# Kernel optimization log

Measured on AMD Instinct MI355X. Metric: run time of the kernel, lower is better.

The kernel has to match this reference:

```python
import jax, jax.numpy as jnp
import numpy as np

H = 1024       # hidden_size
NH = 16        # num heads
HD = H // NH   # head dim
EPS = 1e-12


def setup_inputs() -> dict:
    key = jax.random.key(0)
    ks = jax.random.split(key, 12)
    s = 1.0 / np.sqrt(H)
    return {
        "hidden_states": jax.random.normal(ks[0], (2, 2048, H), jnp.float32),
        "attention_mask": jnp.zeros((2, 1, 1, 2048), jnp.float32),
        "wq": jax.random.uniform(ks[1], (H, H), jnp.float32, -s, s),
        "bq": jnp.zeros((H,), jnp.float32),
        "wk": jax.random.uniform(ks[2], (H, H), jnp.float32, -s, s),
        "bk": jnp.zeros((H,), jnp.float32),
        "wv": jax.random.uniform(ks[3], (H, H), jnp.float32, -s, s),
        "bv": jnp.zeros((H,), jnp.float32),
        "wo": jax.random.uniform(ks[4], (H, H), jnp.float32, -s, s),
        "bo": jnp.zeros((H,), jnp.float32),
        "ln_gamma": jnp.ones((H,), jnp.float32),
        "ln_beta": jnp.zeros((H,), jnp.float32),
    }


def reference(hidden_states, attention_mask, wq, bq, wk, bk, wv, bv, wo, bo, ln_gamma, ln_beta):
    residual = hidden_states
    # pre-LayerNorm
    mu = jnp.mean(hidden_states, axis=-1, keepdims=True)
    var = jnp.var(hidden_states, axis=-1, keepdims=True)
    x = (hidden_states - mu) / jnp.sqrt(var + EPS) * ln_gamma + ln_beta

    B, S, _ = x.shape
    # QKV projections (torch Linear: x @ W.T + b), split heads -> [B, NH, S, HD]
    def proj(w, b):
        return (x @ w.T + b).reshape(B, S, NH, HD).transpose(0, 2, 1, 3)
    q = proj(wq, bq)
    k = proj(wk, bk)
    v = proj(wv, bv)

    scores = jnp.einsum("bhqd,bhkd->bhqk", q, k) / np.sqrt(HD).astype(np.float32)
    scores = scores + attention_mask  # broadcast additive mask
    probs = jax.nn.softmax(scores, axis=-1)
    ctx = jnp.einsum("bhqk,bhkd->bhqd", probs, v)
    ctx = ctx.transpose(0, 2, 1, 3).reshape(B, S, NH * HD)

    out = ctx @ wo.T + bo
    return out + residual
```

## Files before the change

### kernel.cpp

```cpp
#include <hip/hip_runtime.h>
#include <cstdint>

typedef unsigned short u16;
typedef __bf16  bf16x8 __attribute__((ext_vector_type(8)));
typedef unsigned short u16x8 __attribute__((ext_vector_type(8)));
typedef unsigned short u16x4 __attribute__((ext_vector_type(4)));
typedef float   f32x4  __attribute__((ext_vector_type(4)));

#define LOG2E 1.44269504088896340736f

__device__ __forceinline__ u16 f2b(float f) {
  union { __bf16 h; u16 u; } c; c.h = (__bf16)f;
  return c.u;
}

__device__ __forceinline__ int swz(int row) { return (row & 7) ^ ((row >> 3) & 7); }
__device__ __forceinline__ int sidx(int row, int k) {
  return row * 64 + ((((k >> 3) ^ swz(row)) & 7) << 3) + (k & 7);
}
__device__ __forceinline__ bf16x8 ld_frag(const u16* base, int row, int k) {
  return *(const bf16x8*)(base + sidx(row, k));
}

__device__ __forceinline__ void async16(const u16* g, u16* l) {
  __builtin_amdgcn_global_load_lds(
      (__attribute__((address_space(1))) unsigned int*)(uintptr_t)g,
      (__attribute__((address_space(3))) unsigned int*)(uintptr_t)l,
      16, 0, 0);
}

__device__ __forceinline__ void plswap32(unsigned int &a, unsigned int &b) {
  auto r = __builtin_amdgcn_permlane32_swap(a, b, false, false);
  a = r[0]; b = r[1];
}
__device__ __forceinline__ void plswap16(unsigned int &a, unsigned int &b) {
#if __has_builtin(__builtin_amdgcn_permlane16_swap)
  auto r = __builtin_amdgcn_permlane16_swap(a, b, false, false);
  a = r[0]; b = r[1];
#else
  asm volatile("v_permlane16_swap_b32 %0, %1" : "+v"(a), "+v"(b));
#endif
}

__global__ __launch_bounds__(256) void prep_kernel(
    const float* __restrict__ hs, const float* __restrict__ gamma,
    const float* __restrict__ beta, u16* __restrict__ X,
    const float* __restrict__ w0, const float* __restrict__ w1,
    const float* __restrict__ w2, const float* __restrict__ w3,
    u16* __restrict__ Wd) {
  const int tid = threadIdx.x;
  if (blockIdx.x >= 4096) {
    const int idx4 = blockIdx.x - 4096;
    const int mat = idx4 >> 10;
    const float* src = (mat == 0) ? w0 : (mat == 1) ? w1 : (mat == 2) ? w2 : w3;
    const int idx = ((idx4 & 1023) * 256 + tid) * 4;
    f32x4 v = *(const f32x4*)(src + idx);
    u16x4 o;
#pragma unroll
    for (int j = 0; j < 4; ++j) o[j] = f2b(v[j]);
    *(u16x4*)(Wd + (size_t)mat * 1048576 + idx) = o;
    return;
  }
  __shared__ float red[8];
  const int row = blockIdx.x;
  f32x4 v = *(const f32x4*)(hs + (size_t)row * 1024 + tid * 4);
  float s = 0.f, s2 = 0.f;
#pragma unroll
  for (int j = 0; j < 4; ++j) { s += v[j]; s2 += v[j] * v[j]; }
#pragma unroll
  for (int o = 1; o < 64; o <<= 1) { s += __shfl_xor(s, o); s2 += __shfl_xor(s2, o); }
  const int wid = tid >> 6, lane = tid & 63;
  if (lane == 0) { red[wid] = s; red[4 + wid] = s2; }
  __syncthreads();
  s  = red[0] + red[1] + red[2] + red[3];
  s2 = red[4] + red[5] + red[6] + red[7];
  const float mean = s * (1.f / 1024.f);
  const float var  = fmaxf(s2 * (1.f / 1024.f) - mean * mean, 0.f);
  const float rstd = rsqrtf(var + 1e-12f);
  f32x4 g = *(const f32x4*)(gamma + tid * 4);
  f32x4 bb = *(const f32x4*)(beta + tid * 4);
  u16x4 outv;
#pragma unroll
  for (int j = 0; j < 4; ++j) outv[j] = f2b((v[j] - mean) * rstd * g[j] + bb[j]);
  *(u16x4*)(X + (size_t)row * 1024 + tid * 4) = outv;
}

template <int MODE>
__device__ __forceinline__ void gemm_tile_128(
    const u16* __restrict__ A, const u16* __restrict__ Bt,
    const float* __restrict__ bias, const float* __restrict__ res,
    void* __restrict__ Cv, int ldc, int m0, int nG) {
  __shared__ __align__(16) u16 As[128 * 64];
  __shared__ __align__(16) u16 Bs[128 * 64];
  const int tid = threadIdx.x;
  const int wid = tid >> 6;
  const int lane = tid & 63;
  const int l15 = lane & 15, lq = lane >> 4;
  const int wm = (wid & 1) << 6, wn = (wid >> 1) << 6;
  const int srow = tid >> 3;
  const int sg = tid & 7;

  f32x4 acc[4][4] = {};
  u16x8 ar[4], br[4];

#pragma unroll
  for (int i = 0; i < 4; ++i) {
    int row = (i << 5) + srow;
    ar[i] = *(const u16x8*)(A  + (size_t)row * 1024 + (sg << 3));
    br[i] = *(const u16x8*)(Bt + (size_t)row * 1024 + (sg << 3));
  }

  for (int k0 = 0; k0 < 1024; k0 += 64) {
    if (k0) __syncthreads();
#pragma unroll
    for (int i = 0; i < 4; ++i) {
      int row = (i << 5) + srow;
      *(u16x8*)(As + sidx(row, sg << 3)) = ar[i];
      *(u16x8*)(Bs + sidx(row, sg << 3)) = br[i];
    }
    __syncthreads();
    if (k0 + 64 < 1024) {
#pragma unroll
      for (int i = 0; i < 4; ++i) {
        int row = (i << 5) + srow;
        ar[i] = *(const u16x8*)(A  + (size_t)row * 1024 + k0 + 64 + (sg << 3));
        br[i] = *(const u16x8*)(Bt + (size_t)row * 1024 + k0 + 64 + (sg << 3));
      }
    }
#pragma unroll
    for (int kk = 0; kk < 2; ++kk) {
      bf16x8 af[4], bf[4];
#pragma unroll
      for (int mi = 0; mi < 4; ++mi) af[mi] = ld_frag(As, wm + (mi << 4) + l15, (kk << 5) + (lq << 3));
#pragma unroll
      for (int ni = 0; ni < 4; ++ni) bf[ni] = ld_frag(Bs, wn + (ni << 4) + l15, (kk << 5) + (lq << 3));
#pragma unroll
      for (int mi = 0; mi < 4; ++mi)
#pragma unroll
        for (int ni = 0; ni < 4; ++ni)
          acc[mi][ni] = __builtin_amdgcn_mfma_f32_16x16x32_bf16(af[mi], bf[ni], acc[mi][ni], 0, 0, 0);
    }
  }
  __syncthreads();

  if (MODE == 2) {
    u16* Rg = (wid < 2 ? As : Bs) + ((wid & 1) << 12);
#pragma unroll
    for (int ni = 0; ni < 4; ++ni) {
      const float bv = bias[wn + (ni << 4) + l15];
#pragma unroll
      for (int mi = 0; mi < 4; ++mi) {
        u16x4 pk;
#pragma unroll
        for (int r = 0; r < 4; ++r) pk[r] = f2b(acc[mi][ni][r] + bv);
        *(u16x4*)(Rg + sidx((ni << 4) + l15, (mi << 4) + (lq << 2))) = pk;
      }
    }
    __asm__ volatile("" ::: "memory");
    const int rrow = lane >> 3;
    const int rg8  = (lane & 7) << 3;
    const int mg0 = m0 + wm;
    const int bb = mg0 >> 11, ss0 = mg0 & 2047;
    const int hh = (nG + wn) >> 6;
    u16* vbase = (u16*)Cv + ((size_t)((bb << 4) + hh) * 64) * 2048 + ss0;
#pragma unroll
    for (int p = 0; p < 8; ++p) {
      const int nl = (p << 3) + rrow;
      bf16x8 rowv = ld_frag(Rg, nl, rg8);
      *(bf16x8*)(vbase + (size_t)nl * 2048 + rg8) = rowv;
    }
  } else {
#pragma unroll
    for (int ni = 0; ni < 4; ++ni) {
      const int n = wn + (ni << 4) + l15;
      const float bv = bias[n];
#pragma unroll
      for (int mi = 0; mi < 4; ++mi) {
#pragma unroll
        for (int r = 0; r < 4; ++r) {
          const int m = wm + (mi << 4) + (lq << 2) + r;
          float v = acc[mi][ni][r] + bv;
          if (MODE == 1) {
            v += res[(size_t)m * ldc + n];
            ((float*)Cv)[(size_t)m * ldc + n] = v;
          } else {
            ((u16*)Cv)[(size_t)m * ldc + n] = f2b(v);
          }
        }
      }
    }
  }
}

__global__ __launch_bounds__(256, 3) void qkv_kernel(
    const u16* __restrict__ X, const u16* __restrict__ W,
    const float* __restrict__ bq, const float* __restrict__ bk, const float* __restrict__ bv,
    u16* __restrict__ QK, u16* __restrict__ VT) {
  const int n0 = blockIdx.x << 7;
  const int m0 = blockIdx.y << 7;
  const int wsel = n0 >> 10;
  const int nloc = n0 & 1023;
  const u16* Bt = W + (size_t)wsel * 1048576 + (size_t)nloc * 1024;
  if (wsel < 2) {
    const float* bias = (wsel == 0 ? bq : bk) + nloc;
    gemm_tile_128<0>(X + (size_t)m0 * 1024, Bt, bias, nullptr,
                     QK + (size_t)m0 * 2048 + n0, 2048, 0, 0);
  } else {
    gemm_tile_128<2>(X + (size_t)m0 * 1024, Bt, bv + nloc, nullptr,
                     VT, 0, m0, nloc);
  }
}

__global__ __launch_bounds__(256, 3) void out_kernel(
    const u16* __restrict__ CTX, const u16* __restrict__ wo,
    const float* __restrict__ bo, const float* __restrict__ res, float* __restrict__ OUT) {
  const int n0 = blockIdx.x << 7;
  const int m0 = blockIdx.y << 7;
  gemm_tile_128<1>(CTX + (size_t)m0 * 1024, wo + (size_t)n0 * 1024, bo + n0,
                   res + (size_t)m0 * 1024 + n0, OUT + (size_t)m0 * 1024 + n0, 1024, 0, 0);
}

__global__ __launch_bounds__(256, 2) void attn_kernel(
    const u16* __restrict__ QK, const u16* __restrict__ VT,
    const float* __restrict__ mask, u16* __restrict__ CTX) {
  __shared__ __align__(16) u16 Ksb[2][64 * 64];
  __shared__ __align__(16) u16 Vtsb[2][64 * 64];
  const int tid = threadIdx.x;
  const int wid = tid >> 6;
  const int lane = tid & 63;
  const int l15 = lane & 15, lq = lane >> 4;

  const int lid = blockIdx.x;
  const int sw = ((lid & 7) << 6) | (lid >> 3);
  const int qt = sw & 15;
  const int hz = sw >> 4;
  const int h = hz & 15;
  const int b = hz >> 4;

  const int qbase = (b << 11) + (qt << 7) + (wid << 5);
  const u16* Kbase  = QK + (size_t)(b << 11) * 2048 + 1024 + (h << 6);
  const u16* VTbase = VT + (size_t)(((b << 4) + h) << 6) * 2048;

  bf16x8 qf[2][2];
#pragma unroll
  for (int f = 0; f < 2; ++f)
#pragma unroll
    for (int kc = 0; kc < 2; ++kc)
      qf[f][kc] = *(const bf16x8*)(QK + (size_t)(qbase + (f << 4) + l15) * 2048 + (h << 6) + (kc << 5) + (lq << 3));

  f32x4 cacc[2][4] = {};
  float l_run[2] = {0.f, 0.f};

  const int sg = lane & 7;
  const int srow0 = (wid << 4) + (lane >> 3);
  const int srow1 = srow0 + 8;
  const int gk0 = ((sg ^ swz(srow0)) & 7) << 3;
  const int gk1 = ((sg ^ swz(srow1)) & 7) << 3;
  const int ld0 = ((wid << 1) + 0) << 9;
  const int ld1 = ((wid << 1) + 1) << 9;

  async16(Kbase + (size_t)srow0 * 2048 + gk0, &Ksb[0][0] + ld0);
  async16(Kbase + (size_t)srow1 * 2048 + gk1, &Ksb[0][0] + ld1);
  async16(VTbase + (size_t)srow0 * 2048 + gk0, &Vtsb[0][0] + ld0);
  async16(VTbase + (size_t)srow1 * 2048 + gk1, &Vtsb[0][0] + ld1);

  for (int kt = 0; kt < 32; ++kt) {
    const u16* Ks  = &Ksb[kt & 1][0];
    const u16* Vts = &Vtsb[kt & 1][0];
    __syncthreads();
    if (kt + 1 < 32) {
      const int nk = (kt + 1) << 6;
      async16(Kbase + (size_t)(nk + srow0) * 2048 + gk0, &Ksb[(kt + 1) & 1][0] + ld0);
      async16(Kbase + (size_t)(nk + srow1) * 2048 + gk1, &Ksb[(kt + 1) & 1][0] + ld1);
      async16(VTbase + (size_t)srow0 * 2048 + nk + gk0, &Vtsb[(kt + 1) & 1][0] + ld0);
      async16(VTbase + (size_t)srow1 * 2048 + nk + gk1, &Vtsb[(kt + 1) & 1][0] + ld1);
    }

    f32x4 sacc[2][4] = {};
    __builtin_amdgcn_s_setprio(1);
#pragma unroll
    for (int kc = 0; kc < 2; ++kc) {
      bf16x8 kf[4];
#pragma unroll
      for (int ki = 0; ki < 4; ++ki) kf[ki] = ld_frag(Ks, (ki << 4) + l15, (kc << 5) + (lq << 3));
#pragma unroll
      for (int f = 0; f < 2; ++f)
#pragma unroll
        for (int ki = 0; ki < 4; ++ki)
          sacc[f][ki] = __builtin_amdgcn_mfma_f32_16x16x32_bf16(kf[ki], qf[f][kc], sacc[f][ki], 0, 0, 0);
    }
    __builtin_amdgcn_s_setprio(0);

    f32x4 mvl[4];
#pragma unroll
    for (int ki = 0; ki < 4; ++ki) {
      f32x4 mv = *(const f32x4*)(mask + (b << 11) + (kt << 6) + (ki << 4) + (lq << 2));
#pragma unroll
      for (int r = 0; r < 4; ++r) mvl[ki][r] = mv[r] * LOG2E;
    }

    unsigned int w0[2][4], w1[2][4];
#pragma unroll
    for (int f = 0; f < 2; ++f) {
      float rs = 0.f;
#pragma unroll
      for (int ki = 0; ki < 4; ++ki) {
#pragma unroll
        for (int r = 0; r < 4; ++r) {
          float pv = __builtin_amdgcn_exp2f(sacc[f][ki][r] * (0.125f * LOG2E) + mvl[ki][r]);
          sacc[f][ki][r] = pv;
          rs += pv;
        }
        unsigned int wa, wb;
        asm("v_cvt_pk_bf16_f32 %0, %1, %2" : "=v"(wa) : "v"(sacc[f][ki][0]), "v"(sacc[f][ki][1]));
        asm("v_cvt_pk_bf16_f32 %0, %1, %2" : "=v"(wb) : "v"(sacc[f][ki][2]), "v"(sacc[f][ki][3]));
        w0[f][ki] = wa; w1[f][ki] = wb;
      }
      l_run[f] += rs;
    }

#pragma unroll
    for (int kc = 0; kc < 2; ++kc) {
      bf16x8 pf[2];
#pragma unroll
      for (int f = 0; f < 2; ++f) {
        unsigned int a0 = w0[f][(kc << 1) + 0], a1 = w1[f][(kc << 1) + 0];
        unsigned int b0 = w0[f][(kc << 1) + 1], b1 = w1[f][(kc << 1) + 1];
        plswap32(a0, b0); plswap32(a1, b1);
        plswap16(a0, b0); plswap16(a1, b1);
        union { unsigned int u[4]; bf16x8 v; } pc;
        pc.u[0] = a0; pc.u[1] = a1; pc.u[2] = b0; pc.u[3] = b1;
        pf[f] = pc.v;
      }
      __builtin_amdgcn_s_setprio(1);
#pragma unroll
      for (int dm = 0; dm < 4; ++dm) {
        bf16x8 vf = ld_frag(Vts, (dm << 4) + l15, (kc << 5) + (lq << 3));
#pragma unroll
        for (int f = 0; f < 2; ++f)
          cacc[f][dm] = __builtin_amdgcn_mfma_f32_16x16x32_bf16(vf, pf[f], cacc[f][dm], 0, 0, 0);
      }
      __builtin_amdgcn_s_setprio(0);
    }
  }

#pragma unroll
  for (int f = 0; f < 2; ++f) {
    float rs = l_run[f];
    rs += __shfl_xor(rs, 16);
    rs += __shfl_xor(rs, 32);
    const float inv = 1.0f / rs;
    u16* Crow = CTX + (size_t)(qbase + (f << 4) + l15) * 1024 + (h << 6);
#pragma unroll
    for (int dm = 0; dm < 4; ++dm) {
      u16x4 o;
#pragma unroll
      for (int r = 0; r < 4; ++r) o[r] = f2b(cacc[f][dm][r] * inv);
      *(u16x4*)(Crow + (dm << 4) + (lq << 2)) = o;
    }
  }
}

extern "C" void kernel_launch(void* const* d_in, const int* in_sizes, int n_in,
                              void* d_out, int out_size, void* d_ws, size_t ws_size,
                              hipStream_t stream) {
  const float* hs   = (const float*)d_in[0];
  const float* mask = (const float*)d_in[1];
  const float* wq   = (const float*)d_in[2];
  const float* bq   = (const float*)d_in[3];
  const float* wk   = (const float*)d_in[4];
  const float* bk   = (const float*)d_in[5];
  const float* wv   = (const float*)d_in[6];
  const float* bv   = (const float*)d_in[7];
  const float* wo   = (const float*)d_in[8];
  const float* bo   = (const float*)d_in[9];
  const float* lg   = (const float*)d_in[10];
  const float* lb   = (const float*)d_in[11];

  u16* X   = (u16*)d_ws;
  u16* QK  = X + (size_t)4096 * 1024;
  u16* CTX = QK + (size_t)4096 * 2048;
  u16* W   = CTX + (size_t)4096 * 1024;
  u16* VT  = W + (size_t)4 * 1048576;
  float* OUT = (float*)d_out;

  prep_kernel<<<8192, 256, 0, stream>>>(hs, lg, lb, X, wq, wk, wv, wo, W);
  qkv_kernel<<<dim3(24, 32), 256, 0, stream>>>(X, W, bq, bk, bv, QK, VT);
  attn_kernel<<<dim3(512), 256, 0, stream>>>(QK, VT, mask, CTX);
  out_kernel<<<dim3(8, 32), 256, 0, stream>>>(CTX, W + (size_t)3 * 1048576, bo, hs, OUT);
}
```

Measured before the change: 204.5 us.

## Use async global-to-LDS loads in GEMM tile and XCD-aware block remap

The shared GEMM tile routine now loads A and B straight from global memory into LDS with async16 transfers, applying the swizzle on the global side. This replaces the register-staged prefetch, which cuts register pressure and VGPR-to-LDS store instructions. The price is that the next tile is no longer prefetched while the current one computes, so each iteration waits on its load. Separately, the QKV kernel moves to a 1D grid whose block index is remapped so that blocks on the same XCD share rows and columns of the inputs, for better L2 reuse.

```diff
diff --git a/kernel.cpp b/kernel.cpp
--- a/kernel.cpp
+++ b/kernel.cpp
@@ -97,36 +97,26 @@
   const int lane = tid & 63;
   const int l15 = lane & 15, lq = lane >> 4;
   const int wm = (wid & 1) << 6, wn = (wid >> 1) << 6;
-  const int srow = tid >> 3;
-  const int sg = tid & 7;
+  const int lrow = lane >> 3, sg = lane & 7;
+
+  int goff[4];
+#pragma unroll
+  for (int i = 0; i < 4; ++i) {
+    const int row = (wid << 5) + (i << 3) + lrow;
+    goff[i] = row * 1024 + (((sg ^ swz(row)) & 7) << 3);
+  }
 
   f32x4 acc[4][4] = {};
-  u16x8 ar[4], br[4];
-
-#pragma unroll
-  for (int i = 0; i < 4; ++i) {
-    int row = (i << 5) + srow;
-    ar[i] = *(const u16x8*)(A  + (size_t)row * 1024 + (sg << 3));
-    br[i] = *(const u16x8*)(Bt + (size_t)row * 1024 + (sg << 3));
-  }
 
   for (int k0 = 0; k0 < 1024; k0 += 64) {
     if (k0) __syncthreads();
 #pragma unroll
-    for (int i = 0; i < 4; ++i) {
-      int row = (i << 5) + srow;
-      *(u16x8*)(As + sidx(row, sg << 3)) = ar[i];
-      *(u16x8*)(Bs + sidx(row, sg << 3)) = br[i];
-    }
+    for (int i = 0; i < 4; ++i)
+      async16(A + goff[i] + k0, As + (((wid << 5) + (i << 3)) << 6));
+#pragma unroll
+    for (int i = 0; i < 4; ++i)
+      async16(Bt + goff[i] + k0, Bs + (((wid << 5) + (i << 3)) << 6));
     __syncthreads();
-    if (k0 + 64 < 1024) {
-#pragma unroll
-      for (int i = 0; i < 4; ++i) {
-        int row = (i << 5) + srow;
-        ar[i] = *(const u16x8*)(A  + (size_t)row * 1024 + k0 + 64 + (sg << 3));
-        br[i] = *(const u16x8*)(Bt + (size_t)row * 1024 + k0 + 64 + (sg << 3));
-      }
-    }
 #pragma unroll
     for (int kk = 0; kk < 2; ++kk) {
       bf16x8 af[4], bf[4];
@@ -196,8 +186,12 @@
     const u16* __restrict__ X, const u16* __restrict__ W,
     const float* __restrict__ bq, const float* __restrict__ bk, const float* __restrict__ bv,
     u16* __restrict__ QK, u16* __restrict__ VT) {
-  const int n0 = blockIdx.x << 7;
-  const int m0 = blockIdx.y << 7;
+  const int lid = blockIdx.x;
+  const int xcd = lid & 7, idx = lid >> 3;
+  const int by = ((xcd >> 1) << 3) + (idx & 7);
+  const int bx = (xcd & 1) * 12 + (idx >> 3);
+  const int n0 = bx << 7;
+  const int m0 = by << 7;
   const int wsel = n0 >> 10;
   const int nloc = n0 & 1023;
   const u16* Bt = W + (size_t)wsel * 1048576 + (size_t)nloc * 1024;
@@ -385,7 +379,7 @@
   float* OUT = (float*)d_out;
 
   prep_kernel<<<8192, 256, 0, stream>>>(hs, lg, lb, X, wq, wk, wv, wo, W);
-  qkv_kernel<<<dim3(24, 32), 256, 0, stream>>>(X, W, bq, bk, bv, QK, VT);
+  qkv_kernel<<<dim3(768), 256, 0, stream>>>(X, W, bq, bk, bv, QK, VT);
   attn_kernel<<<dim3(512), 256, 0, stream>>>(QK, VT, mask, CTX);
   out_kernel<<<dim3(8, 32), 256, 0, stream>>>(CTX, W + (size_t)3 * 1048576, bo, hs, OUT);
 }
```

After: 216.6 us. +5.9%, slower.

## Double-buffer QKV GEMM with async LDS loads and compute softmax sums via MFMA

Applied to the files above, without the earlier changes.

The QKV projection GEMM moves to a new tile routine that double-buffers A and B tiles in LDS using async global-to-LDS copies, so the next K-slice loads while the current one is multiplied. This doubles shared memory per block and lowers the occupancy hint from 3 to 2. The output GEMM keeps the old register-staged path, now specialised to the residual-add epilogue. In attention, the per-row softmax denominator is now accumulated with an extra MFMA against a ones vector instead of scalar adds and cross-lane shuffles. That uses bf16-rounded probabilities, which also makes the denominator consistent with the numerator.

```diff
diff --git a/kernel.cpp b/kernel.cpp
--- a/kernel.cpp
+++ b/kernel.cpp
@@ -89,7 +89,7 @@
 __device__ __forceinline__ void gemm_tile_128(
     const u16* __restrict__ A, const u16* __restrict__ Bt,
     const float* __restrict__ bias, const float* __restrict__ res,
-    void* __restrict__ Cv, int ldc, int m0, int nG) {
+    void* __restrict__ Cv, int ldc) {
   __shared__ __align__(16) u16 As[128 * 64];
   __shared__ __align__(16) u16 Bs[128 * 64];
   const int tid = threadIdx.x;
@@ -141,10 +141,82 @@
           acc[mi][ni] = __builtin_amdgcn_mfma_f32_16x16x32_bf16(af[mi], bf[ni], acc[mi][ni], 0, 0, 0);
     }
   }
+
+#pragma unroll
+  for (int ni = 0; ni < 4; ++ni) {
+    const int n = wn + (ni << 4) + l15;
+    const float bv = bias[n];
+#pragma unroll
+    for (int mi = 0; mi < 4; ++mi) {
+#pragma unroll
+      for (int r = 0; r < 4; ++r) {
+        const int m = wm + (mi << 4) + (lq << 2) + r;
+        float v = acc[mi][ni][r] + bv;
+        v += res[(size_t)m * ldc + n];
+        ((float*)Cv)[(size_t)m * ldc + n] = v;
+      }
+    }
+  }
+}
+
+template <int MODE>
+__device__ __forceinline__ void gemm_tile_128_gl(
+    const u16* __restrict__ A, const u16* __restrict__ Bt,
+    const float* __restrict__ bias,
+    void* __restrict__ Cv, int ldc, int m0, int nG) {
+  __shared__ __align__(16) u16 Asb[2][128 * 64];
+  __shared__ __align__(16) u16 Bsb[2][128 * 64];
+  const int tid = threadIdx.x;
+  const int wid = tid >> 6;
+  const int lane = tid & 63;
+  const int l15 = lane & 15, lq = lane >> 4;
+  const int wm = (wid & 1) << 6, wn = (wid >> 1) << 6;
+  const int lrow = lane >> 3, sg = lane & 7;
+
+  int goff[4], kld[4];
+#pragma unroll
+  for (int i = 0; i < 4; ++i) {
+    const int row = (wid << 5) + (i << 3) + lrow;
+    goff[i] = row * 1024 + (((sg ^ swz(row)) & 7) << 3);
+    kld[i] = ((wid << 5) + (i << 3)) << 6;
+  }
+
+  f32x4 acc[4][4] = {};
+
+#pragma unroll
+  for (int i = 0; i < 4; ++i) async16(A  + goff[i], &Asb[0][0] + kld[i]);
+#pragma unroll
+  for (int i = 0; i < 4; ++i) async16(Bt + goff[i], &Bsb[0][0] + kld[i]);
+
+  for (int k0 = 0; k0 < 1024; k0 += 64) {
+    const int buf = (k0 >> 6) & 1;
+    __syncthreads();
+    if (k0 + 64 < 1024) {
+#pragma unroll
+      for (int i = 0; i < 4; ++i) async16(A  + goff[i] + k0 + 64, &Asb[buf ^ 1][0] + kld[i]);
+#pragma unroll
+      for (int i = 0; i < 4; ++i) async16(Bt + goff[i] + k0 + 64, &Bsb[buf ^ 1][0] + kld[i]);
+    }
+    const u16* As = &Asb[buf][0];
+    const u16* Bs = &Bsb[buf][0];
+#pragma unroll
+    for (int kk = 0; kk < 2; ++kk) {
+      bf16x8 af[4], bf[4];
+#pragma unroll
+      for (int mi = 0; mi < 4; ++mi) af[mi] = ld_frag(As, wm + (mi << 4) + l15, (kk << 5) + (lq << 3));
+#pragma unroll
+      for (int ni = 0; ni < 4; ++ni) bf[ni] = ld_frag(Bs, wn + (ni << 4) + l15, (kk << 5) + (lq << 3));
+#pragma unroll
+      for (int mi = 0; mi < 4; ++mi)
+#pragma unroll
+        for (int ni = 0; ni < 4; ++ni)
+          acc[mi][ni] = __builtin_amdgcn_mfma_f32_16x16x32_bf16(af[mi], bf[ni], acc[mi][ni], 0, 0, 0);
+    }
+  }
   __syncthreads();
 
   if (MODE == 2) {
-    u16* Rg = (wid < 2 ? As : Bs) + ((wid & 1) << 12);
+    u16* Rg = (wid < 2 ? &Asb[0][0] : &Bsb[0][0]) + ((wid & 1) << 12);
 #pragma unroll
     for (int ni = 0; ni < 4; ++ni) {
       const float bv = bias[wn + (ni << 4) + l15];
@@ -179,20 +251,14 @@
 #pragma unroll
         for (int r = 0; r < 4; ++r) {
           const int m = wm + (mi << 4) + (lq << 2) + r;
-          float v = acc[mi][ni][r] + bv;
-          if (MODE == 1) {
-            v += res[(size_t)m * ldc + n];
-            ((float*)Cv)[(size_t)m * ldc + n] = v;
-          } else {
-            ((u16*)Cv)[(size_t)m * ldc + n] = f2b(v);
-          }
+          ((u16*)Cv)[(size_t)m * ldc + n] = f2b(acc[mi][ni][r] + bv);
         }
       }
     }
   }
 }
 
-__global__ __launch_bounds__(256, 3) void qkv_kernel(
+__global__ __launch_bounds__(256, 2) void qkv_kernel(
     const u16* __restrict__ X, const u16* __restrict__ W,
     const float* __restrict__ bq, const float* __restrict__ bk, const float* __restrict__ bv,
     u16* __restrict__ QK, u16* __restrict__ VT) {
@@ -203,11 +269,11 @@
   const u16* Bt = W + (size_t)wsel * 1048576 + (size_t)nloc * 1024;
   if (wsel < 2) {
     const float* bias = (wsel == 0 ? bq : bk) + nloc;
-    gemm_tile_128<0>(X + (size_t)m0 * 1024, Bt, bias, nullptr,
-                     QK + (size_t)m0 * 2048 + n0, 2048, 0, 0);
+    gemm_tile_128_gl<0>(X + (size_t)m0 * 1024, Bt, bias,
+                        QK + (size_t)m0 * 2048 + n0, 2048, 0, 0);
   } else {
-    gemm_tile_128<2>(X + (size_t)m0 * 1024, Bt, bv + nloc, nullptr,
-                     VT, 0, m0, nloc);
+    gemm_tile_128_gl<2>(X + (size_t)m0 * 1024, Bt, bv + nloc,
+                        VT, 0, m0, nloc);
   }
 }
 
@@ -217,7 +283,7 @@
   const int n0 = blockIdx.x << 7;
   const int m0 = blockIdx.y << 7;
   gemm_tile_128<1>(CTX + (size_t)m0 * 1024, wo + (size_t)n0 * 1024, bo + n0,
-                   res + (size_t)m0 * 1024 + n0, OUT + (size_t)m0 * 1024 + n0, 1024, 0, 0);
+                   res + (size_t)m0 * 1024 + n0, OUT + (size_t)m0 * 1024 + n0, 1024);
 }
 
 __global__ __launch_bounds__(256, 2) void attn_kernel(
@@ -248,8 +314,12 @@
     for (int kc = 0; kc < 2; ++kc)
       qf[f][kc] = *(const bf16x8*)(QK + (size_t)(qbase + (f << 4) + l15) * 2048 + (h << 6) + (kc << 5) + (lq << 3));
 
+  bf16x8 onesf;
+#pragma unroll
+  for (int j = 0; j < 8; ++j) onesf[j] = (__bf16)1.0f;
+
   f32x4 cacc[2][4] = {};
-  float l_run[2] = {0.f, 0.f};
+  f32x4 lacc[2] = {};
 
   const int sg = lane & 7;
   const int srow0 = (wid << 4) + (lane >> 3);
@@ -302,21 +372,16 @@
     unsigned int w0[2][4], w1[2][4];
 #pragma unroll
     for (int f = 0; f < 2; ++f) {
-      float rs = 0.f;
 #pragma unroll
       for (int ki = 0; ki < 4; ++ki) {
 #pragma unroll
-        for (int r = 0; r < 4; ++r) {
-          float pv = __builtin_amdgcn_exp2f(sacc[f][ki][r] * (0.125f * LOG2E) + mvl[ki][r]);
-          sacc[f][ki][r] = pv;
-          rs += pv;
-        }
+        for (int r = 0; r < 4; ++r)
+          sacc[f][ki][r] = __builtin_amdgcn_exp2f(sacc[f][ki][r] * (0.125f * LOG2E) + mvl[ki][r]);
         unsigned int wa, wb;
         asm("v_cvt_pk_bf16_f32 %0, %1, %2" : "=v"(wa) : "v"(sacc[f][ki][0]), "v"(sacc[f][ki][1]));
         asm("v_cvt_pk_bf16_f32 %0, %1, %2" : "=v"(wb) : "v"(sacc[f][ki][2]), "v"(sacc[f][ki][3]));
         w0[f][ki] = wa; w1[f][ki] = wb;
       }
-      l_run[f] += rs;
     }
 
 #pragma unroll
@@ -340,16 +405,16 @@
         for (int f = 0; f < 2; ++f)
           cacc[f][dm] = __builtin_amdgcn_mfma_f32_16x16x32_bf16(vf, pf[f], cacc[f][dm], 0, 0, 0);
       }
+#pragma unroll
+      for (int f = 0; f < 2; ++f)
+        lacc[f] = __builtin_amdgcn_mfma_f32_16x16x32_bf16(onesf, pf[f], lacc[f], 0, 0, 0);
       __builtin_amdgcn_s_setprio(0);
     }
   }
 
 #pragma unroll
   for (int f = 0; f < 2; ++f) {
-    float rs = l_run[f];
-    rs += __shfl_xor(rs, 16);
-    rs += __shfl_xor(rs, 32);
-    const float inv = 1.0f / rs;
+    const float inv = 1.0f / lacc[f][0];
     u16* Crow = CTX + (size_t)(qbase + (f << 4) + l15) * 1024 + (h << 6);
 #pragma unroll
     for (int dm = 0; dm < 4; ++dm) {
```

Result: slower. 209.8 us (+2.6%).

## Software-pipeline attention loop with 4-stage buffers and MFMA row-sum

Applied to the files above, without the earlier changes.

Restructures the attention kernel's K/V loop into a two-tile ping-pong so that the QK MFMAs for the next tile are issued alongside the softmax and PV MFMAs of the current tile. Shared-memory K/V buffers grow from double to quad buffering with three tiles prefetched ahead. The per-row softmax denominator is now accumulated by an extra MFMA against a vector of ones, which replaces the scalar adds and cross-lane shuffles. The cost is doubled LDS use and higher register pressure, which could reduce occupancy. The denominator now sums the bf16-rounded probabilities, so results differ slightly from before.

```diff
diff --git a/kernel.cpp b/kernel.cpp
--- a/kernel.cpp
+++ b/kernel.cpp
@@ -220,11 +220,90 @@
                    res + (size_t)m0 * 1024 + n0, OUT + (size_t)m0 * 1024 + n0, 1024, 0, 0);
 }
 
+__device__ __forceinline__ void qk_tile(const u16* Ks, const bf16x8 (&qf)[2][2],
+                                        f32x4 (&sacc)[2][4], int l15, int lq) {
+  f32x4 z = {};
+#pragma unroll
+  for (int f = 0; f < 2; ++f)
+#pragma unroll
+    for (int ki = 0; ki < 4; ++ki) sacc[f][ki] = z;
+  __builtin_amdgcn_s_setprio(1);
+#pragma unroll
+  for (int kc = 0; kc < 2; ++kc) {
+    bf16x8 kf[4];
+#pragma unroll
+    for (int ki = 0; ki < 4; ++ki) kf[ki] = ld_frag(Ks, (ki << 4) + l15, (kc << 5) + (lq << 3));
+#pragma unroll
+    for (int f = 0; f < 2; ++f)
+#pragma unroll
+      for (int ki = 0; ki < 4; ++ki)
+        sacc[f][ki] = __builtin_amdgcn_mfma_f32_16x16x32_bf16(kf[ki], qf[f][kc], sacc[f][ki], 0, 0, 0);
+  }
+  __builtin_amdgcn_s_setprio(0);
+}
+
+__device__ __forceinline__ void mask_load(const float* mp, f32x4 (&mvl)[4]) {
+#pragma unroll
+  for (int ki = 0; ki < 4; ++ki) {
+    f32x4 mv = *(const f32x4*)(mp + (ki << 4));
+#pragma unroll
+    for (int r = 0; r < 4; ++r) mvl[ki][r] = mv[r] * LOG2E;
+  }
+}
+
+__device__ __forceinline__ void softmax_pack(f32x4 (&sacc)[2][4], const f32x4 (&mvl)[4],
+                                             unsigned int (&w0)[2][4], unsigned int (&w1)[2][4]) {
+#pragma unroll
+  for (int f = 0; f < 2; ++f) {
+#pragma unroll
+    for (int ki = 0; ki < 4; ++ki) {
+#pragma unroll
+      for (int r = 0; r < 4; ++r)
+        sacc[f][ki][r] = __builtin_amdgcn_exp2f(sacc[f][ki][r] * (0.125f * LOG2E) + mvl[ki][r]);
+      unsigned int wa, wb;
+      asm("v_cvt_pk_bf16_f32 %0, %1, %2" : "=v"(wa) : "v"(sacc[f][ki][0]), "v"(sacc[f][ki][1]));
+      asm("v_cvt_pk_bf16_f32 %0, %1, %2" : "=v"(wb) : "v"(sacc[f][ki][2]), "v"(sacc[f][ki][3]));
+      w0[f][ki] = wa; w1[f][ki] = wb;
+    }
+  }
+}
+
+__device__ __forceinline__ void pv_tile(const u16* Vts, unsigned int (&w0)[2][4],
+                                        unsigned int (&w1)[2][4], f32x4 (&cacc)[2][4],
+                                        f32x4 (&lacc)[2], bf16x8 onesf, int l15, int lq) {
+#pragma unroll
+  for (int kc = 0; kc < 2; ++kc) {
+    bf16x8 pf[2];
+#pragma unroll
+    for (int f = 0; f < 2; ++f) {
+      unsigned int a0 = w0[f][(kc << 1) + 0], a1 = w1[f][(kc << 1) + 0];
+      unsigned int b0 = w0[f][(kc << 1) + 1], b1 = w1[f][(kc << 1) + 1];
+      plswap32(a0, b0); plswap32(a1, b1);
+      plswap16(a0, b0); plswap16(a1, b1);
+      union { unsigned int u[4]; bf16x8 v; } pc;
+      pc.u[0] = a0; pc.u[1] = a1; pc.u[2] = b0; pc.u[3] = b1;
+      pf[f] = pc.v;
+    }
+    __builtin_amdgcn_s_setprio(1);
+#pragma unroll
+    for (int dm = 0; dm < 4; ++dm) {
+      bf16x8 vf = ld_frag(Vts, (dm << 4) + l15, (kc << 5) + (lq << 3));
+#pragma unroll
+      for (int f = 0; f < 2; ++f)
+        cacc[f][dm] = __builtin_amdgcn_mfma_f32_16x16x32_bf16(vf, pf[f], cacc[f][dm], 0, 0, 0);
+    }
+#pragma unroll
+    for (int f = 0; f < 2; ++f)
+      lacc[f] = __builtin_amdgcn_mfma_f32_16x16x32_bf16(onesf, pf[f], lacc[f], 0, 0, 0);
+    __builtin_amdgcn_s_setprio(0);
+  }
+}
+
 __global__ __launch_bounds__(256, 2) void attn_kernel(
     const u16* __restrict__ QK, const u16* __restrict__ VT,
     const float* __restrict__ mask, u16* __restrict__ CTX) {
-  __shared__ __align__(16) u16 Ksb[2][64 * 64];
-  __shared__ __align__(16) u16 Vtsb[2][64 * 64];
+  __shared__ __align__(16) u16 Ksb[4][64 * 64];
+  __shared__ __align__(16) u16 Vtsb[4][64 * 64];
   const int tid = threadIdx.x;
   const int wid = tid >> 6;
   const int lane = tid & 63;
@@ -240,6 +319,7 @@
   const int qbase = (b << 11) + (qt << 7) + (wid << 5);
   const u16* Kbase  = QK + (size_t)(b << 11) * 2048 + 1024 + (h << 6);
   const u16* VTbase = VT + (size_t)(((b << 4) + h) << 6) * 2048;
+  const float* Mbase = mask + (b << 11) + (lq << 2);
 
   bf16x8 qf[2][2];
 #pragma unroll
@@ -248,8 +328,12 @@
     for (int kc = 0; kc < 2; ++kc)
       qf[f][kc] = *(const bf16x8*)(QK + (size_t)(qbase + (f << 4) + l15) * 2048 + (h << 6) + (kc << 5) + (lq << 3));
 
+  bf16x8 onesf;
+#pragma unroll
+  for (int j = 0; j < 8; ++j) onesf[j] = (__bf16)1.0f;
+
   f32x4 cacc[2][4] = {};
-  float l_run[2] = {0.f, 0.f};
+  f32x4 lacc[2] = {};
 
   const int sg = lane & 7;
   const int srow0 = (wid << 4) + (lane >> 3);
@@ -259,97 +343,51 @@
   const int ld0 = ((wid << 1) + 0) << 9;
   const int ld1 = ((wid << 1) + 1) << 9;
 
-  async16(Kbase + (size_t)srow0 * 2048 + gk0, &Ksb[0][0] + ld0);
-  async16(Kbase + (size_t)srow1 * 2048 + gk1, &Ksb[0][0] + ld1);
-  async16(VTbase + (size_t)srow0 * 2048 + gk0, &Vtsb[0][0] + ld0);
-  async16(VTbase + (size_t)srow1 * 2048 + gk1, &Vtsb[0][0] + ld1);
-
-  for (int kt = 0; kt < 32; ++kt) {
-    const u16* Ks  = &Ksb[kt & 1][0];
-    const u16* Vts = &Vtsb[kt & 1][0];
+  auto STAGE = [&](int t) {
+    u16* kb = &Ksb[t & 3][0];
+    u16* vb = &Vtsb[t & 3][0];
+    const int nk = t << 6;
+    async16(Kbase + (size_t)(nk + srow0) * 2048 + gk0, kb + ld0);
+    async16(Kbase + (size_t)(nk + srow1) * 2048 + gk1, kb + ld1);
+    async16(VTbase + (size_t)srow0 * 2048 + nk + gk0, vb + ld0);
+    async16(VTbase + (size_t)srow1 * 2048 + nk + gk1, vb + ld1);
+  };
+
+  STAGE(0); STAGE(1); STAGE(2);
+  __syncthreads();
+
+  f32x4 saccA[2][4], saccB[2][4];
+  f32x4 mvlA[4], mvlB[4];
+  qk_tile(&Ksb[0][0], qf, saccA, l15, lq);
+  mask_load(Mbase, mvlA);
+
+  for (int i = 0; i < 16; ++i) {
+    const int e = i << 1;
+    if (e + 3 < 32) STAGE(e + 3);
+    mask_load(Mbase + ((e + 1) << 6), mvlB);
+    {
+      unsigned int w0[2][4], w1[2][4];
+      softmax_pack(saccA, mvlA, w0, w1);
+      qk_tile(&Ksb[(e + 1) & 3][0], qf, saccB, l15, lq);
+      pv_tile(&Vtsb[e & 3][0], w0, w1, cacc, lacc, onesf, l15, lq);
+    }
     __syncthreads();
-    if (kt + 1 < 32) {
-      const int nk = (kt + 1) << 6;
-      async16(Kbase + (size_t)(nk + srow0) * 2048 + gk0, &Ksb[(kt + 1) & 1][0] + ld0);
-      async16(Kbase + (size_t)(nk + srow1) * 2048 + gk1, &Ksb[(kt + 1) & 1][0] + ld1);
-      async16(VTbase + (size_t)srow0 * 2048 + nk + gk0, &Vtsb[(kt + 1) & 1][0] + ld0);
-      async16(VTbase + (size_t)srow1 * 2048 + nk + gk1, &Vtsb[(kt + 1) & 1][0] + ld1);
-    }
-
-    f32x4 sacc[2][4] = {};
-    __builtin_amdgcn_s_setprio(1);
-#pragma unroll
-    for (int kc = 0; kc < 2; ++kc) {
-      bf16x8 kf[4];
-#pragma unroll
-      for (int ki = 0; ki < 4; ++ki) kf[ki] = ld_frag(Ks, (ki << 4) + l15, (kc << 5) + (lq << 3));
-#pragma unroll
-      for (int f = 0; f < 2; ++f)
-#pragma unroll
-        for (int ki = 0; ki < 4; ++ki)
-          sacc[f][ki] = __builtin_amdgcn_mfma_f32_16x16x32_bf16(kf[ki], qf[f][kc], sacc[f][ki], 0, 0, 0);
-    }
-    __builtin_amdgcn_s_setprio(0);
-
-    f32x4 mvl[4];
-#pragma unroll
-    for (int ki = 0; ki < 4; ++ki) {
-      f32x4 mv = *(const f32x4*)(mask + (b << 11) + (kt << 6) + (ki << 4) + (lq << 2));
-#pragma unroll
-      for (int r = 0; r < 4; ++r) mvl[ki][r] = mv[r] * LOG2E;
-    }
-
-    unsigned int w0[2][4], w1[2][4];
-#pragma unroll
-    for (int f = 0; f < 2; ++f) {
-      float rs = 0.f;
-#pragma unroll
-      for (int ki = 0; ki < 4; ++ki) {
-#pragma unroll
-        for (int r = 0; r < 4; ++r) {
-          float pv = __builtin_amdgcn_exp2f(sacc[f][ki][r] * (0.125f * LOG2E) + mvl[ki][r]);
-          sacc[f][ki][r] = pv;
-          rs += pv;
-        }
-        unsigned int wa, wb;
-        asm("v_cvt_pk_bf16_f32 %0, %1, %2" : "=v"(wa) : "v"(sacc[f][ki][0]), "v"(sacc[f][ki][1]));
-        asm("v_cvt_pk_bf16_f32 %0, %1, %2" : "=v"(wb) : "v"(sacc[f][ki][2]), "v"(sacc[f][ki][3]));
-        w0[f][ki] = wa; w1[f][ki] = wb;
-      }
-      l_run[f] += rs;
-    }
-
-#pragma unroll
-    for (int kc = 0; kc < 2; ++kc) {
-      bf16x8 pf[2];
-#pragma unroll
-      for (int f = 0; f < 2; ++f) {
-        unsigned int a0 = w0[f][(kc << 1) + 0], a1 = w1[f][(kc << 1) + 0];
-        unsigned int b0 = w0[f][(kc << 1) + 1], b1 = w1[f][(kc << 1) + 1];
-        plswap32(a0, b0); plswap32(a1, b1);
-        plswap16(a0, b0); plswap16(a1, b1);
-        union { unsigned int u[4]; bf16x8 v; } pc;
-        pc.u[0] = a0; pc.u[1] = a1; pc.u[2] = b0; pc.u[3] = b1;
-        pf[f] = pc.v;
-      }
-      __builtin_amdgcn_s_setprio(1);
-#pragma unroll
-      for (int dm = 0; dm < 4; ++dm) {
-        bf16x8 vf = ld_frag(Vts, (dm << 4) + l15, (kc << 5) + (lq << 3));
-#pragma unroll
-        for (int f = 0; f < 2; ++f)
-          cacc[f][dm] = __builtin_amdgcn_mfma_f32_16x16x32_bf16(vf, pf[f], cacc[f][dm], 0, 0, 0);
-      }
-      __builtin_amdgcn_s_setprio(0);
-    }
+
+    const int o = e + 1;
+    if (o + 3 < 32) STAGE(o + 3);
+    if (o < 31) mask_load(Mbase + ((o + 1) << 6), mvlA);
+    {
+      unsigned int w0[2][4], w1[2][4];
+      softmax_pack(saccB, mvlB, w0, w1);
+      if (o < 31) qk_tile(&Ksb[(o + 1) & 3][0], qf, saccA, l15, lq);
+      pv_tile(&Vtsb[o & 3][0], w0, w1, cacc, lacc, onesf, l15, lq);
+    }
+    __syncthreads();
   }
 
 #pragma unroll
   for (int f = 0; f < 2; ++f) {
-    float rs = l_run[f];
-    rs += __shfl_xor(rs, 16);
-    rs += __shfl_xor(rs, 32);
-    const float inv = 1.0f / rs;
+    const float inv = 1.0f / lacc[f][0];
     u16* Crow = CTX + (size_t)(qbase + (f << 4) + l15) * 1024 + (h << 6);
 #pragma unroll
     for (int dm = 0; dm < 4; ++dm) {
```

Result: no change. 200.6 us (-1.9%).
